# Kernel tuning notes

Measured on AMD Instinct MI355X. Metric: run time of the kernel, lower is better.

Reference implementation:

```python
import jax, jax.numpy as jnp
import numpy as np

D_K = 64
D_MODEL = 1024
SEQ = 4096
BATCH = 4


def setup_inputs() -> dict:
    key = jax.random.key(0)
    ks = jax.random.split(key, 7)
    s = 1.0 / np.sqrt(D_MODEL)
    return {
        "x": jax.random.normal(ks[0], (BATCH, SEQ, D_MODEL), dtype=jnp.float32),
        "wq": jax.random.uniform(ks[1], (D_K, D_MODEL), jnp.float32, -s, s),
        "bq": jax.random.uniform(ks[2], (D_K,), jnp.float32, -s, s),
        "wk": jax.random.uniform(ks[3], (D_K, D_MODEL), jnp.float32, -s, s),
        "bk": jax.random.uniform(ks[4], (D_K,), jnp.float32, -s, s),
        "wv": jax.random.uniform(ks[5], (D_K, D_MODEL), jnp.float32, -s, s),
        "bv": jax.random.uniform(ks[6], (D_K,), jnp.float32, -s, s),
    }


def reference(x, wq, bq, wk, bk, wv, bv):
    # q,k,v: [B,T,d_k]
    q = jnp.einsum('btc,dc->btd', x, wq) + bq
    k = jnp.einsum('btc,dc->btd', x, wk) + bk
    v = jnp.einsum('btc,dc->btd', x, wv) + bv
    scale = 1.0 / np.sqrt(D_K).astype(np.float32)
    scores = jnp.einsum('bqd,bkd->bqk', q, k) * scale  # [B,T,T]
    T = x.shape[1]
    causal = jnp.tril(jnp.ones((T, T), dtype=bool))
    scores = jnp.where(causal, scores, -jnp.inf)
    sm = jax.nn.softmax(scores, axis=-1)
    return jnp.einsum('bqk,bkd->bqd', sm, v)
```

## Files before the change

kernel.cpp:

```cpp
#include <hip/hip_runtime.h>

typedef __attribute__((ext_vector_type(8))) short short8;
typedef __attribute__((ext_vector_type(4))) float f32x4;

#define D_KV   64
#define SEQ    4096
#define NBATCH 4
#define DMODEL 1024

static __device__ __forceinline__ unsigned short f32_to_bf16(float f) {
  unsigned u = __builtin_bit_cast(unsigned, f);
  u = (u + 0x7FFFu + ((u >> 16) & 1u)) >> 16;
  return (unsigned short)u;
}

static __device__ __forceinline__ void gload_lds16(const void* gsrc, void* ldst) {
  __builtin_amdgcn_global_load_lds(
      (const __attribute__((address_space(1))) void*)gsrc,
      (__attribute__((address_space(3))) void*)ldst, 16, 0, 0);
}

__global__ __launch_bounds__(256) void wcvt_kernel(
    const float* __restrict__ wq, const float* __restrict__ wk,
    const float* __restrict__ wv, unsigned short* __restrict__ wfrag) {
  const int fid = blockIdx.x * 256 + threadIdx.x;
  const int nt = fid >> 11, ks = (fid >> 6) & 31, lane = fid & 63;
  const int l16 = lane & 15, lq = lane >> 4;
  const float* w = (nt < 4) ? wq : (nt < 8) ? wk : wv;
  const float* src = w + ((nt & 3) * 16 + l16) * DMODEL + ks * 32 + lq * 8;
  short8 v;
#pragma unroll
  for (int j = 0; j < 8; ++j) v[j] = (short)f32_to_bf16(src[j]);
  *reinterpret_cast<short8*>(wfrag + (long)fid * 8) = v;
}

__global__ __launch_bounds__(256) void qkv_proj_kernel(
    const float* __restrict__ x, const unsigned short* __restrict__ wfrag,
    const float* __restrict__ bq, const float* __restrict__ bk,
    const float* __restrict__ bv,
    unsigned short* __restrict__ Qf, unsigned short* __restrict__ Kf,
    unsigned short* __restrict__ Vf) {
  __shared__ __align__(16) float lds_x[2 * 32 * 128];
  const int tid = threadIdx.x, lane = tid & 63, wave = tid >> 6;
  const int l16 = lane & 15, lq = lane >> 4;
  const long rowbase = (long)blockIdx.x * 32;
  unsigned char* lx = (unsigned char*)lds_x;
  const unsigned char* xb = (const unsigned char*)x;

  f32x4 acc[3][2];
#pragma unroll
  for (int i = 0; i < 3; ++i)
#pragma unroll
    for (int s = 0; s < 2; ++s) acc[i][s] = (f32x4){0.f, 0.f, 0.f, 0.f};

  const unsigned short* wbase = wfrag + (long)(3 * wave) * 16384 + lane * 8;

#define STAGE(ck, buf)                                                        \
  {                                                                           \
    _Pragma("unroll")                                                         \
    for (int i = 0; i < 4; ++i) {                                             \
      const int slot = wave * 4 + i;                           \
      const int pos = slot * 1024 + lane * 16;                                \
      const int row = pos >> 9;                                               \
      const int colb = (pos & 511) ^ ((row & 7) << 4);                        \
      gload_lds16(xb + ((rowbase + row) << 12) + (ck) * 512 + colb,           \
                  lx + (buf) * 16384 + slot * 1024);                          \
    }                                                                         \
  }

  STAGE(0, 0);
  __syncthreads();

  for (int ck = 0; ck < 8; ++ck) {
    const int cur = ck & 1;
    if (ck < 7) STAGE(ck + 1, cur ^ 1);
    const int curoff = cur * 16384;
#pragma unroll
    for (int ks = 0; ks < 4; ++ks) {
      short8 a[2];
#pragma unroll
      for (int sub = 0; sub < 2; ++sub) {
        const int row = sub * 16 + l16;
        const int swz = (row & 7) << 4;
        const unsigned char* rp = lx + curoff + row * 512;
        const f32x4 f0 = *reinterpret_cast<const f32x4*>(
            rp + ((ks * 128 + lq * 32) ^ swz));
        const f32x4 f1 = *reinterpret_cast<const f32x4*>(
            rp + ((ks * 128 + lq * 32 + 16) ^ swz));
#pragma unroll
        for (int j = 0; j < 4; ++j) {
          a[sub][j]     = (short)f32_to_bf16(f0[j]);
          a[sub][4 + j] = (short)f32_to_bf16(f1[j]);
        }
      }
#pragma unroll
      for (int i = 0; i < 3; ++i) {
        const short8 b = *reinterpret_cast<const short8*>(
            wbase + (long)i * 16384 + (ck * 4 + ks) * 512);
        acc[i][0] = __builtin_amdgcn_mfma_f32_16x16x32_bf16(a[0], b, acc[i][0], 0, 0, 0);
        acc[i][1] = __builtin_amdgcn_mfma_f32_16x16x32_bf16(a[1], b, acc[i][1], 0, 0, 0);
      }
    }
    __syncthreads();
  }

#pragma unroll
  for (int i = 0; i < 3; ++i) {
    const int nt = 3 * wave + i;
    const int mat = nt >> 2;
    const int dcol = ((nt & 3) << 4) | l16;
    const float bias = (mat == 0 ? bq : mat == 1 ? bk : bv)[dcol];
    const int c = dcol >> 5, lqp = (dcol >> 3) & 3, jj = dcol & 7;
#pragma unroll
    for (int sub = 0; sub < 2; ++sub)
#pragma unroll
      for (int rr = 0; rr < 4; ++rr) {
        const long t = rowbase + sub * 16 + lq * 4 + rr;
        const float sum = acc[i][sub][rr] + bias;
        if (mat == 0) {
          Qf[(((t >> 4) * 2 + c) * 64 + lqp * 16 + (t & 15)) * 8 + jj] =
              f32_to_bf16(sum * 0.125f);
        } else if (mat == 1) {
          Kf[((((t >> 6) * 4 + ((t >> 4) & 3)) * 2 + c) * 64 + lqp * 16 +
              (t & 15)) * 8 + jj] = f32_to_bf16(sum);
        } else {
          Vf[((((t >> 6) * 4 + (dcol >> 4)) * 2 + ((t >> 5) & 1)) * 64 +
              ((t >> 3) & 3) * 16 + (dcol & 15)) * 8 + (t & 7)] =
              f32_to_bf16(sum);
        }
      }
  }
#undef STAGE
}

__global__ __launch_bounds__(256) void attn_kernel(
    const unsigned short* __restrict__ Qf, const unsigned short* __restrict__ Kf,
    const unsigned short* __restrict__ Vf, float* __restrict__ out) {
  __shared__ __align__(16) unsigned short p_lds[4][16][72];
  __shared__ __align__(16) float lds_o[4][16][68];
  __shared__ float lds_ml[4][16][2];
  __shared__ float lds_gl[16];

  const int tid = threadIdx.x;
  const int lane = tid & 63;
  const int wave = tid >> 6;
  const int l16 = lane & 15, lq = lane >> 4;
  const int b = blockIdx.y;
  const int tile = 255 - blockIdx.x;
  const int qbase = tile * 16;
  const long qrow = (long)b * SEQ + qbase;

  short8 qf[2];
#pragma unroll
  for (int c = 0; c < 2; ++c)
    qf[c] = *reinterpret_cast<const short8*>(
        Qf + ((qrow >> 4) * 2 + c) * 512 + lane * 8);

  f32x4 o[4];
#pragma unroll
  for (int dt = 0; dt < 4; ++dt) o[dt] = (f32x4){0.f, 0.f, 0.f, 0.f};
  float m = -INFINITY, ell = 0.f;

  const long ktile0 = (long)b * 64;
  const int nkv = qbase / 64 + 1;
  for (int kt = wave; kt < nkv; kt += 4) {
    const int kvbase = kt * 64;
    const unsigned short* kb = Kf + (ktile0 + kt) * 4096 + lane * 8;
    const unsigned short* vb = Vf + (ktile0 + kt) * 4096 + lane * 8;
    f32x4 s[4];
#pragma unroll
    for (int ct = 0; ct < 4; ++ct) s[ct] = (f32x4){0.f, 0.f, 0.f, 0.f};
#pragma unroll
    for (int ct = 0; ct < 4; ++ct)
#pragma unroll
      for (int c = 0; c < 2; ++c) {
        short8 kf = *reinterpret_cast<const short8*>(kb + (ct * 2 + c) * 512);
        s[ct] = __builtin_amdgcn_mfma_f32_16x16x32_bf16(kf, qf[c], s[ct], 0, 0, 0);
      }
    if (kt == nkv - 1) {
      const int qg = qbase + l16;
#pragma unroll
      for (int ct = 0; ct < 4; ++ct)
#pragma unroll
        for (int r = 0; r < 4; ++r)
          if (kvbase + ct * 16 + lq * 4 + r > qg) s[ct][r] = -INFINITY;
    }
    float mx = -INFINITY;
#pragma unroll
    for (int ct = 0; ct < 4; ++ct)
#pragma unroll
      for (int r = 0; r < 4; ++r) mx = fmaxf(mx, s[ct][r]);
    mx = fmaxf(mx, __shfl_xor(mx, 16, 64));
    mx = fmaxf(mx, __shfl_xor(mx, 32, 64));
    const float nm = fmaxf(m, mx);
    const float alpha = __expf(m - nm);
    float rs = 0.f;
#pragma unroll
    for (int ct = 0; ct < 4; ++ct)
#pragma unroll
      for (int r = 0; r < 4; ++r) {
        const float p = __expf(s[ct][r] - nm);
        s[ct][r] = p;
        rs += p;
      }
    rs += __shfl_xor(rs, 16, 64);
    rs += __shfl_xor(rs, 32, 64);
    ell = ell * alpha + rs;
    m = nm;
#pragma unroll
    for (int dt = 0; dt < 4; ++dt) o[dt] *= alpha;
#pragma unroll
    for (int ct = 0; ct < 4; ++ct)
#pragma unroll
      for (int r = 0; r < 4; ++r)
        p_lds[wave][l16][ct * 16 + lq * 4 + r] = f32_to_bf16(s[ct][r]);
    short8 pf[2];
#pragma unroll
    for (int c = 0; c < 2; ++c)
      pf[c] = *reinterpret_cast<const short8*>(&p_lds[wave][l16][c * 32 + lq * 8]);
#pragma unroll
    for (int dt = 0; dt < 4; ++dt)
#pragma unroll
      for (int c = 0; c < 2; ++c) {
        short8 vf = *reinterpret_cast<const short8*>(vb + (dt * 2 + c) * 512);
        o[dt] = __builtin_amdgcn_mfma_f32_16x16x32_bf16(vf, pf[c], o[dt], 0, 0, 0);
      }
  }

  if (lane < 16) {
    lds_ml[wave][l16][0] = m;
    lds_ml[wave][l16][1] = ell;
  }
  __syncthreads();
  const float m0 = lds_ml[0][l16][0], m1 = lds_ml[1][l16][0];
  const float m2 = lds_ml[2][l16][0], m3 = lds_ml[3][l16][0];
  const float g = fmaxf(fmaxf(m0, m1), fmaxf(m2, m3));
  const float gl = lds_ml[0][l16][1] * __expf(m0 - g) +
                   lds_ml[1][l16][1] * __expf(m1 - g) +
                   lds_ml[2][l16][1] * __expf(m2 - g) +
                   lds_ml[3][l16][1] * __expf(m3 - g);
  const float myscale = __expf(m - g);
  if (wave == 0 && lane < 16) lds_gl[l16] = gl;
#pragma unroll
  for (int dt = 0; dt < 4; ++dt)
#pragma unroll
    for (int r = 0; r < 4; ++r)
      lds_o[wave][l16][dt * 16 + lq * 4 + r] = o[dt][r] * myscale;
  __syncthreads();
#pragma unroll
  for (int j = 0; j < 4; ++j) {
    const int e = tid + 256 * j;
    const int row = e >> 6, col = e & 63;
    const float sum = lds_o[0][row][col] + lds_o[1][row][col] +
                      lds_o[2][row][col] + lds_o[3][row][col];
    out[(qrow + row) * D_KV + col] = sum / lds_gl[row];
  }
}

extern "C" void kernel_launch(void* const* d_in, const int* in_sizes, int n_in,
                              void* d_out, int out_size, void* d_ws, size_t ws_size,
                              hipStream_t stream) {
  const float* x  = (const float*)d_in[0];
  const float* wq = (const float*)d_in[1];
  const float* bq = (const float*)d_in[2];
  const float* wk = (const float*)d_in[3];
  const float* bk = (const float*)d_in[4];
  const float* wv = (const float*)d_in[5];
  const float* bv = (const float*)d_in[6];
  float* out = (float*)d_out;

  unsigned short* ws    = (unsigned short*)d_ws;
  unsigned short* wfrag = ws;
  unsigned short* Qf    = ws + 196608;
  unsigned short* Kf    = Qf + 1048576;
  unsigned short* Vf    = Kf + 1048576;

  wcvt_kernel<<<96, 256, 0, stream>>>(wq, wk, wv, wfrag);
  qkv_proj_kernel<<<512, 256, 0, stream>>>(x, wfrag, bq, bk, bv, Qf, Kf, Vf);
  dim3 ag(256, NBATCH);
  attn_kernel<<<ag, 256, 0, stream>>>(Qf, Kf, Vf, out);
}
```

Before: 74.69 us.

## Preload full x tile as bf16 into LDS and register-prefetch weight fragments

The QKV projection kernel no longer double-buffers fp32 x chunks with global_load_lds. It now loads the whole 32x1024 row tile once through registers, converts it to bf16 and stores it swizzled in LDS (64KB), which removes the per-chunk barriers and the repeated fp32->bf16 conversion in the inner loop. Weight fragments are prefetched one chunk ahead into registers. The trade-off is higher LDS and register use (launch_bounds 256,1), which lowers occupancy, and there is no overlap between the upfront global load and compute.

After: 65.47 us. 1.14x faster.

```diff
diff --git a/kernel.cpp b/kernel.cpp
--- a/kernel.cpp
+++ b/kernel.cpp
@@ -12,12 +12,6 @@
   unsigned u = __builtin_bit_cast(unsigned, f);
   u = (u + 0x7FFFu + ((u >> 16) & 1u)) >> 16;
   return (unsigned short)u;
-}
-
-static __device__ __forceinline__ void gload_lds16(const void* gsrc, void* ldst) {
-  __builtin_amdgcn_global_load_lds(
-      (const __attribute__((address_space(1))) void*)gsrc,
-      (__attribute__((address_space(3))) void*)ldst, 16, 0, 0);
 }
 
 __global__ __launch_bounds__(256) void wcvt_kernel(
@@ -34,18 +28,51 @@
   *reinterpret_cast<short8*>(wfrag + (long)fid * 8) = v;
 }
 
-__global__ __launch_bounds__(256) void qkv_proj_kernel(
+__global__ __launch_bounds__(256, 1) void qkv_proj_kernel(
     const float* __restrict__ x, const unsigned short* __restrict__ wfrag,
     const float* __restrict__ bq, const float* __restrict__ bk,
     const float* __restrict__ bv,
     unsigned short* __restrict__ Qf, unsigned short* __restrict__ Kf,
     unsigned short* __restrict__ Vf) {
-  __shared__ __align__(16) float lds_x[2 * 32 * 128];
+  __shared__ __align__(16) unsigned short lds_x[32 * 1024];
   const int tid = threadIdx.x, lane = tid & 63, wave = tid >> 6;
   const int l16 = lane & 15, lq = lane >> 4;
   const long rowbase = (long)blockIdx.x * 32;
   unsigned char* lx = (unsigned char*)lds_x;
-  const unsigned char* xb = (const unsigned char*)x;
+
+  {
+    const int srow = tid >> 3, scol = (tid & 7) * 16;
+    const float* xrow = x + (rowbase + srow) * DMODEL + scol;
+    const int swz = (srow & 7) << 4;
+    unsigned char* lbase = lx + srow * 2048;
+#pragma unroll
+    for (int s = 0; s < 8; ++s) {
+      const f32x4 f0 = *reinterpret_cast<const f32x4*>(xrow + s * 128);
+      const f32x4 f1 = *reinterpret_cast<const f32x4*>(xrow + s * 128 + 4);
+      const f32x4 f2 = *reinterpret_cast<const f32x4*>(xrow + s * 128 + 8);
+      const f32x4 f3 = *reinterpret_cast<const f32x4*>(xrow + s * 128 + 12);
+      short8 s0, s1;
+#pragma unroll
+      for (int j = 0; j < 4; ++j) {
+        s0[j]     = (short)f32_to_bf16(f0[j]);
+        s0[4 + j] = (short)f32_to_bf16(f1[j]);
+        s1[j]     = (short)f32_to_bf16(f2[j]);
+        s1[4 + j] = (short)f32_to_bf16(f3[j]);
+      }
+      const int bcol = scol * 2 + s * 256;
+      *reinterpret_cast<short8*>(lbase + (bcol ^ swz)) = s0;
+      *reinterpret_cast<short8*>(lbase + ((bcol + 16) ^ swz)) = s1;
+    }
+  }
+  __syncthreads();
+
+  const unsigned short* wbase = wfrag + (long)(3 * wave) * 16384 + lane * 8;
+
+  short8 bw[12];
+#pragma unroll
+  for (int j = 0; j < 12; ++j)
+    bw[j] = *reinterpret_cast<const short8*>(
+        wbase + (long)(j >> 2) * 16384 + (j & 3) * 512);
 
   f32x4 acc[3][2];
 #pragma unroll
@@ -53,55 +80,38 @@
 #pragma unroll
     for (int s = 0; s < 2; ++s) acc[i][s] = (f32x4){0.f, 0.f, 0.f, 0.f};
 
-  const unsigned short* wbase = wfrag + (long)(3 * wave) * 16384 + lane * 8;
-
-#define STAGE(ck, buf)                                                        \
-  {                                                                           \
-    _Pragma("unroll")                                                         \
-    for (int i = 0; i < 4; ++i) {                                             \
-      const int slot = wave * 4 + i;                           \
-      const int pos = slot * 1024 + lane * 16;                                \
-      const int row = pos >> 9;                                               \
-      const int colb = (pos & 511) ^ ((row & 7) << 4);                        \
-      gload_lds16(xb + ((rowbase + row) << 12) + (ck) * 512 + colb,           \
-                  lx + (buf) * 16384 + slot * 1024);                          \
-    }                                                                         \
-  }
-
-  STAGE(0, 0);
-  __syncthreads();
-
+#pragma unroll
   for (int ck = 0; ck < 8; ++ck) {
-    const int cur = ck & 1;
-    if (ck < 7) STAGE(ck + 1, cur ^ 1);
-    const int curoff = cur * 16384;
-#pragma unroll
-    for (int ks = 0; ks < 4; ++ks) {
-      short8 a[2];
+    short8 bn[12];
+    if (ck < 7) {
+#pragma unroll
+      for (int j = 0; j < 12; ++j)
+        bn[j] = *reinterpret_cast<const short8*>(
+            wbase + (long)(j >> 2) * 16384 + ((ck + 1) * 4 + (j & 3)) * 512);
+    }
+    short8 a[4][2];
+#pragma unroll
+    for (int kc = 0; kc < 4; ++kc)
 #pragma unroll
       for (int sub = 0; sub < 2; ++sub) {
         const int row = sub * 16 + l16;
-        const int swz = (row & 7) << 4;
-        const unsigned char* rp = lx + curoff + row * 512;
-        const f32x4 f0 = *reinterpret_cast<const f32x4*>(
-            rp + ((ks * 128 + lq * 32) ^ swz));
-        const f32x4 f1 = *reinterpret_cast<const f32x4*>(
-            rp + ((ks * 128 + lq * 32 + 16) ^ swz));
-#pragma unroll
-        for (int j = 0; j < 4; ++j) {
-          a[sub][j]     = (short)f32_to_bf16(f0[j]);
-          a[sub][4 + j] = (short)f32_to_bf16(f1[j]);
-        }
-      }
+        a[kc][sub] = *reinterpret_cast<const short8*>(
+            lx + row * 2048 +
+            (((ck * 4 + kc) * 64 + lq * 16) ^ ((row & 7) << 4)));
+      }
+#pragma unroll
+    for (int kc = 0; kc < 4; ++kc)
 #pragma unroll
       for (int i = 0; i < 3; ++i) {
-        const short8 b = *reinterpret_cast<const short8*>(
-            wbase + (long)i * 16384 + (ck * 4 + ks) * 512);
-        acc[i][0] = __builtin_amdgcn_mfma_f32_16x16x32_bf16(a[0], b, acc[i][0], 0, 0, 0);
-        acc[i][1] = __builtin_amdgcn_mfma_f32_16x16x32_bf16(a[1], b, acc[i][1], 0, 0, 0);
-      }
-    }
-    __syncthreads();
+        acc[i][0] = __builtin_amdgcn_mfma_f32_16x16x32_bf16(
+            a[kc][0], bw[i * 4 + kc], acc[i][0], 0, 0, 0);
+        acc[i][1] = __builtin_amdgcn_mfma_f32_16x16x32_bf16(
+            a[kc][1], bw[i * 4 + kc], acc[i][1], 0, 0, 0);
+      }
+    if (ck < 7) {
+#pragma unroll
+      for (int j = 0; j < 12; ++j) bw[j] = bn[j];
+    }
   }
 
 #pragma unroll
@@ -130,7 +140,6 @@
         }
       }
   }
-#undef STAGE
 }
 
 __global__ __launch_bounds__(256) void attn_kernel(
```
